# Kernel tuning notes

Measured on AMD Instinct MI355X. Metric: run time of the kernel, lower is better.

The kernel has to match this reference:

```python
import jax, jax.numpy as jnp
import numpy as np

EMBED_DIM = 1024
NUM_HEADS = 16
BATCH = 4
SEQ = 2048
HEAD_DIM = EMBED_DIM // NUM_HEADS


def get_alibi_slope(num_heads):
    x = (2 ** 8) ** (1 / num_heads)
    slope = jnp.array([1 / x ** (i + 1) for i in range(num_heads)], dtype=jnp.float32)
    return slope[:, None, None]  # [H,1,1]


def setup_inputs() -> dict:
    key = jax.random.key(0)
    k1, k2, k3 = jax.random.split(key, 3)
    x = jax.random.normal(k1, (BATCH, SEQ, EMBED_DIM), dtype=jnp.float32)
    # causal mask, broadcastable to [B,H,S,S]
    mask = jnp.tril(jnp.ones((SEQ, SEQ), dtype=bool))[None, None, :, :]
    W_qkv = jax.random.normal(k2, (EMBED_DIM, 3 * EMBED_DIM), dtype=jnp.float32) * (EMBED_DIM ** -0.5)
    b_qkv = jnp.zeros((3 * EMBED_DIM,), dtype=jnp.float32)
    W_out = jax.random.normal(k3, (EMBED_DIM, EMBED_DIM), dtype=jnp.float32) * (EMBED_DIM ** -0.5)
    b_out = jnp.zeros((EMBED_DIM,), dtype=jnp.float32)
    return {"x": x, "mask": mask, "W_qkv": W_qkv, "b_qkv": b_qkv, "W_out": W_out, "b_out": b_out}


def reference(x, mask, W_qkv, b_qkv, W_out, b_out):
    B, S, E = x.shape
    H, D = NUM_HEADS, HEAD_DIM
    qkv = x @ W_qkv + b_qkv                     # [B,S,3E]
    qkv = qkv.reshape(B, S, 3, H, D)
    q, k, v = qkv[:, :, 0], qkv[:, :, 1], qkv[:, :, 2]  # each [B,S,H,D]
    scores = jnp.einsum('bqhd,bkhd->bhqk', q, k) / jnp.sqrt(jnp.asarray(D, x.dtype))
    # ALiBi bias: slope[h] * (k_pos - q_pos)
    rel = (jnp.arange(S)[None, :] - jnp.arange(S)[:, None]).astype(x.dtype)  # [S,S]
    scores = scores + get_alibi_slope(H).astype(x.dtype) * rel               # broadcast [H,S,S]
    scores = jnp.where(mask, scores, jnp.asarray(-1e9, x.dtype))
    attn = jax.nn.softmax(scores, axis=-1)       # [B,H,S,S]
    out = jnp.einsum('bhqk,bkhd->bqhd', attn, v).reshape(B, S, E)
    return out @ W_out + b_out
```

## Files before the change

kernel.cpp:

```cpp
#include <hip/hip_runtime.h>
#include <hip/hip_bf16.h>
#include <cstdint>
#include <cstddef>

#define BATCH  4
#define SEQ    2048
#define EMBED  1024
#define NHEADS 16
#define HDIM   64

typedef __attribute__((ext_vector_type(8))) short  short8;
typedef __attribute__((ext_vector_type(4))) float  floatx4;

#define MASK_NEG (-1.0e30f)
#define LOG2E    1.44269504f

__device__ __forceinline__ float bf2f(ushort u) {
  union { uint32_t i; float f; } v; v.i = ((uint32_t)u) << 16; return v.f;
}
__device__ __forceinline__ ushort f2bf(float f) {
  union { float f; uint32_t i; } v; v.f = f;
  uint32_t u = v.i;
  return (ushort)((u + 0x7fffu + ((u >> 16) & 1u)) >> 16);
}
__device__ __forceinline__ uint32_t f2bf_pk(float a, float b) {
  union { __hip_bfloat162 h; uint32_t u; } v;
  v.h = __float22bfloat162_rn(make_float2(a, b));
  return v.u;
}
__device__ __forceinline__ void gll16(const ushort* g, ushort* l) {
  __builtin_amdgcn_global_load_lds(
      (const __attribute__((address_space(1))) void*)g,
      (__attribute__((address_space(3))) void*)l, 16, 0, 0);
}

__global__ __launch_bounds__(256) void detect_dtype(
    const uint32_t* __restrict__ x, int* __restrict__ flag) {
  __shared__ int sh[256];
  int tid = threadIdx.x;
  int c = 0;
#pragma unroll
  for (int i = 0; i < 16; i++) {
    uint32_t w = x[tid * 16 + i];
    uint32_t lo = w & 0xFFFFu;
    int e = (int)((lo >> 7) & 0xFF);
    if (lo == 0u || (e >= 100 && e <= 140)) c++;
  }
  sh[tid] = c;
  __syncthreads();
  if (tid == 0) {
    int s = 0;
    for (int i = 0; i < 256; i++) s += sh[i];
    *flag = (s >= 3500) ? 1 : 0;
  }
}

__global__ __launch_bounds__(256) void cvt_bf16_v4(
    const void* __restrict__ in, ushort* __restrict__ out,
    const int* __restrict__ flag, int n4) {
  bool isbf = (*flag != 0);
  int stride = gridDim.x * 256;
  for (int i = blockIdx.x * 256 + threadIdx.x; i < n4; i += stride) {
    if (isbf) {
      ((uint2*)out)[i] = ((const uint2*)in)[i];
    } else {
      float4 f = ((const float4*)in)[i];
      uint2 o;
      o.x = f2bf_pk(f.x, f.y);
      o.y = f2bf_pk(f.z, f.w);
      ((uint2*)out)[i] = o;
    }
  }
}

__global__ __launch_bounds__(256) void cvt_biases(
    const void* __restrict__ bq, const void* __restrict__ bo,
    ushort* __restrict__ bqb, ushort* __restrict__ bob,
    const int* __restrict__ flag) {
  bool isbf = (*flag != 0);
  int i = blockIdx.x * 256 + threadIdx.x;
  if (i < 3 * EMBED) {
    bqb[i] = isbf ? ((const ushort*)bq)[i] : f2bf(((const float*)bq)[i]);
  } else {
    int j = i - 3 * EMBED;
    bob[j] = isbf ? ((const ushort*)bo)[j] : f2bf(((const float*)bo)[j]);
  }
}

__global__ __launch_bounds__(256) void transpose_cvt(
    const void* __restrict__ in, ushort* __restrict__ out,
    const int* __restrict__ flag, int R, int C) {
  bool isbf = (*flag != 0);
  __shared__ ushort tile[32][33];
  int bx = blockIdx.x * 32;
  int by = blockIdx.y * 32;
  int tx = threadIdx.x & 31, ty = threadIdx.x >> 5;
#pragma unroll
  for (int i = 0; i < 32; i += 8) {
    size_t idx = (size_t)(by + ty + i) * C + bx + tx;
    tile[ty + i][tx] = isbf ? ((const ushort*)in)[idx] : f2bf(((const float*)in)[idx]);
  }
  __syncthreads();
#pragma unroll
  for (int i = 0; i < 32; i += 8)
    out[(size_t)(bx + ty + i) * R + by + tx] = tile[tx][ty + i];
}

__global__ __launch_bounds__(256) void transpose_v(
    const ushort* __restrict__ in, ushort* __restrict__ out) {
  __shared__ ushort tile[32][33];
  int bh = blockIdx.z;
  int s0 = blockIdx.x * 32;
  int d0 = blockIdx.y * 32;
  int tx = threadIdx.x & 31, ty = threadIdx.x >> 5;
  const ushort* ip = in + (size_t)bh * SEQ * HDIM;
  ushort* op = out + (size_t)bh * SEQ * HDIM;
#pragma unroll
  for (int i = 0; i < 32; i += 8)
    tile[ty + i][tx] = ip[(size_t)(s0 + ty + i) * HDIM + d0 + tx];
  __syncthreads();
#pragma unroll
  for (int i = 0; i < 32; i += 8)
    op[(size_t)(d0 + ty + i) * SEQ + s0 + tx] = tile[tx][ty + i];
}

template <int EPI>
__global__ __launch_bounds__(256) void gemm128(
    const ushort* __restrict__ A, const ushort* __restrict__ BT,
    const ushort* __restrict__ bias,
    ushort* __restrict__ out0, ushort* __restrict__ out1, ushort* __restrict__ out2,
    const int* __restrict__ flag,
    int M, int N, int K) {
  __shared__ __align__(16) ushort Al[128 * 64];
  __shared__ __align__(16) ushort Bl[128 * 64];

  const int tid  = threadIdx.x;
  const int lane = tid & 63, wave = tid >> 6;
  const int quad = lane >> 4, l15 = lane & 15;
  const int wm = wave >> 1, wn = wave & 1;
  const int rowA0 = blockIdx.y * 128;
  const int colB0 = blockIdx.x * 128;

  floatx4 acc[4][4] = {};

  int srow[4], sc8[4];
#pragma unroll
  for (int j = 0; j < 4; j++) {
    int s = tid + j * 256;
    srow[j] = s >> 3;
    sc8[j] = ((s & 7) ^ (srow[j] & 7)) * 8;
  }

  for (int kk = 0; kk < K; kk += 64) {
    __syncthreads();
#pragma unroll
    for (int j = 0; j < 4; j++)
      gll16(&A[(size_t)(rowA0 + srow[j]) * K + kk + sc8[j]], &Al[(tid + j * 256) * 8]);
#pragma unroll
    for (int j = 0; j < 4; j++)
      gll16(&BT[(size_t)(colB0 + srow[j]) * K + kk + sc8[j]], &Bl[(tid + j * 256) * 8]);
    __syncthreads();

#pragma unroll
    for (int h = 0; h < 2; h++) {
      short8 af[4], bf[4];
#pragma unroll
      for (int mt = 0; mt < 4; mt++) {
        int row = wm * 64 + mt * 16 + l15;
        int pos = (quad + 4 * h) ^ (l15 & 7);
        af[mt] = *(const short8*)&Al[row * 64 + pos * 8];
      }
#pragma unroll
      for (int nt = 0; nt < 4; nt++) {
        int row = wn * 64 + nt * 16 + l15;
        int pos = (quad + 4 * h) ^ (l15 & 7);
        bf[nt] = *(const short8*)&Bl[row * 64 + pos * 8];
      }
#pragma unroll
      for (int mt = 0; mt < 4; mt++)
#pragma unroll
        for (int nt = 0; nt < 4; nt++)
          acc[mt][nt] = __builtin_amdgcn_mfma_f32_16x16x32_bf16(af[mt], bf[nt], acc[mt][nt], 0, 0, 0);
    }
  }

  const bool isbf = (EPI == 1) ? (*flag != 0) : true;

#pragma unroll
  for (int mt = 0; mt < 4; mt++)
#pragma unroll
    for (int nt = 0; nt < 4; nt++)
#pragma unroll
      for (int r = 0; r < 4; r++) {
        int row = rowA0 + wm * 64 + mt * 16 + quad * 4 + r;
        int col = colB0 + wn * 64 + nt * 16 + l15;
        float v = acc[mt][nt][r] + bf2f(bias[col]);
        if (EPI == 0) {
          int three = col >> 10, rem = col & 1023, h = rem >> 6, d = rem & 63;
          int b = row >> 11, s = row & 2047;
          ushort* dst = (three == 0) ? out0 : (three == 1) ? out1 : out2;
          dst[((size_t)(b * NHEADS + h) * SEQ + s) * HDIM + d] = f2bf(v);
        } else {
          if (isbf) out0[(size_t)row * N + col] = f2bf(v);
          else      ((float*)out0)[(size_t)row * N + col] = v;
        }
      }
}

__global__ __launch_bounds__(256, 4) void attn_kernel(
    const ushort* __restrict__ Q, const ushort* __restrict__ K,
    const ushort* __restrict__ VT, ushort* __restrict__ Oout) {
  __shared__ __align__(16) ushort Kl[2][64 * 64];
  __shared__ __align__(16) ushort Vt[2][64 * 64];
  __shared__ __align__(16) ushort Pl[4][16 * 64];

  const int tid  = threadIdx.x;
  const int lane = tid & 63, wave = tid >> 6;
  const int quad = lane >> 4, l15 = lane & 15;

  const int L   = blockIdx.x + 16 * blockIdx.y + 256 * blockIdx.z;
  const int xcd = L & 7;
  const int idx = L >> 3;
  const int bh  = xcd * 8 + (idx >> 4);
  const int p   = idx & 15;
  const int h   = bh & 15, b = bh >> 4;

  const ushort* Qp  = Q  + (size_t)bh * SEQ * HDIM;
  const ushort* Kp  = K  + (size_t)bh * SEQ * HDIM;
  const ushort* VTp = VT + (size_t)bh * SEQ * HDIM;

  const float slope2 = exp2f(-0.5f * (float)(h + 1)) * LOG2E;
  const float c2 = 0.125f * LOG2E;
  float rt[4];
#pragma unroll
  for (int r = 0; r < 4; r++) rt[r] = slope2 * (float)r;

  const int sr0 = tid >> 3, sr1 = sr0 + 32;
  const int sc  = tid & 7;
  const int so  = sc * 8;
  const int sw0 = sr0 * 64 + (sc ^ (sr0 & 7)) * 8;
  const int sw1 = sr1 * 64 + (sc ^ (sr0 & 7)) * 8;
  const int sxr = l15 & 7;

  for (int qsel = 0; qsel < 2; qsel++) {
    const int qt  = qsel ? (31 - p) : p;
    const int wq0 = qt * 64 + wave * 16;

    short8 qf0, qf1;
    {
      const ushort* qr = &Qp[(size_t)(wq0 + l15) * HDIM];
      qf0 = *(const short8*)&qr[quad * 8];
      qf1 = *(const short8*)&qr[32 + quad * 8];
    }

    float m2 = MASK_NEG, li = 0.f;
    const float qrowf = (float)(wq0 + l15);
    floatx4 o_acc[4] = {};

    uint4 pk0 = *(const uint4*)&Kp[(size_t)sr0 * HDIM + so];
    uint4 pk1 = *(const uint4*)&Kp[(size_t)sr1 * HDIM + so];
    uint4 pv0 = *(const uint4*)&VTp[(size_t)sr0 * SEQ + so];
    uint4 pv1 = *(const uint4*)&VTp[(size_t)sr1 * SEQ + so];
    __syncthreads();
    *(uint4*)&Kl[0][sw0] = pk0;
    *(uint4*)&Kl[0][sw1] = pk1;
    *(uint4*)&Vt[0][sw0] = pv0;
    *(uint4*)&Vt[0][sw1] = pv1;
    __syncthreads();

    const int ntiles = qt + 1;
    for (int kt = 0; kt < ntiles; kt++) {
      const int kb = kt * 64;
      const int cur = kt & 1;
      const bool more = (kt + 1 < ntiles);

      if (more) {
        const int kb2 = kb + 64;
        pk0 = *(const uint4*)&Kp[(size_t)(kb2 + sr0) * HDIM + so];
        pk1 = *(const uint4*)&Kp[(size_t)(kb2 + sr1) * HDIM + so];
        pv0 = *(const uint4*)&VTp[(size_t)sr0 * SEQ + kb2 + so];
        pv1 = *(const uint4*)&VTp[(size_t)sr1 * SEQ + kb2 + so];
      }

      floatx4 sm[4];
#pragma unroll
      for (int kct = 0; kct < 4; kct++) {
        const ushort* kr = &Kl[cur][(kct * 16 + l15) * 64];
        short8 a0 = *(const short8*)&kr[(quad ^ sxr) * 8];
        short8 a1 = *(const short8*)&kr[((quad + 4) ^ sxr) * 8];
        floatx4 z = {};
        z = __builtin_amdgcn_mfma_f32_16x16x32_bf16(a0, qf0, z, 0, 0, 0);
        sm[kct] = __builtin_amdgcn_mfma_f32_16x16x32_bf16(a1, qf1, z, 0, 0, 0);
      }

      const bool needs_mask = (kb + 63 > wq0);
      float mloc = MASK_NEG;
#pragma unroll
      for (int kct = 0; kct < 4; kct++) {
        float keyb = (float)(kb + kct * 16 + quad * 4);
        float base = slope2 * keyb;
#pragma unroll
        for (int r = 0; r < 4; r++) {
          float v = fmaf(sm[kct][r], c2, base + rt[r]);
          if (needs_mask && (keyb + (float)r > qrowf)) v = MASK_NEG;
          sm[kct][r] = v;
          mloc = fmaxf(mloc, v);
        }
      }
      mloc = fmaxf(mloc, __shfl_xor(mloc, 16, 64));
      mloc = fmaxf(mloc, __shfl_xor(mloc, 32, 64));

      float mn = fmaxf(m2, mloc);
      float al = exp2f(m2 - mn);
      m2 = mn;

      float rs = 0.f;
#pragma unroll
      for (int kct = 0; kct < 4; kct++) {
        float p0 = exp2f(sm[kct][0] - mn), p1 = exp2f(sm[kct][1] - mn);
        float p2 = exp2f(sm[kct][2] - mn), p3 = exp2f(sm[kct][3] - mn);
        rs += (p0 + p1) + (p2 + p3);
        uint2 pw;
        pw.x = f2bf_pk(p0, p1);
        pw.y = f2bf_pk(p2, p3);
        *(uint2*)&Pl[wave][l15 * 64 + ((kct * 2 + (quad >> 1)) ^ sxr) * 8 + (quad & 1) * 4] = pw;
      }
      rs += __shfl_xor(rs, 16, 64);
      rs += __shfl_xor(rs, 32, 64);
      li = li * al + rs;

      float alr[4];
#pragma unroll
      for (int r = 0; r < 4; r++) alr[r] = __shfl(al, quad * 4 + r, 16);
#pragma unroll
      for (int ct = 0; ct < 4; ct++)
#pragma unroll
        for (int r = 0; r < 4; r++) o_acc[ct][r] *= alr[r];

#pragma unroll
      for (int ks = 0; ks < 2; ks++) {
        short8 vf[4];
#pragma unroll
        for (int ct = 0; ct < 4; ct++)
          vf[ct] = *(const short8*)&Vt[cur][(ct * 16 + l15) * 64 + ((ks * 4 + quad) ^ sxr) * 8];
        short8 pf = *(const short8*)&Pl[wave][l15 * 64 + ((ks * 4 + quad) ^ sxr) * 8];
#pragma unroll
        for (int ct = 0; ct < 4; ct++)
          o_acc[ct] = __builtin_amdgcn_mfma_f32_16x16x32_bf16(pf, vf[ct], o_acc[ct], 0, 0, 0);
      }

      if (more) {
        const int nxt = cur ^ 1;
        *(uint4*)&Kl[nxt][sw0] = pk0;
        *(uint4*)&Kl[nxt][sw1] = pk1;
        *(uint4*)&Vt[nxt][sw0] = pv0;
        *(uint4*)&Vt[nxt][sw1] = pv1;
      }
      __syncthreads();
    }

    {
      float inv = 1.0f / fmaxf(li, 1e-20f);
      float invr[4];
#pragma unroll
      for (int r = 0; r < 4; r++) invr[r] = __shfl(inv, quad * 4 + r, 16);
#pragma unroll
      for (int ct = 0; ct < 4; ct++)
#pragma unroll
        for (int r = 0; r < 4; r++) {
          int q = wq0 + quad * 4 + r;
          float v = o_acc[ct][r] * invr[r];
          Oout[(size_t)(b * SEQ + q) * EMBED + h * HDIM + ct * 16 + l15] = f2bf(v);
        }
    }
  }
}

extern "C" void kernel_launch(void* const* d_in, const int* in_sizes, int n_in,
                              void* d_out, int out_size, void* d_ws, size_t ws_size,
                              hipStream_t stream) {
  const void* x     = d_in[0];
  const void* W_qkv = d_in[2];
  const void* b_qkv = d_in[3];
  const void* W_out = d_in[4];
  const void* b_out = d_in[5];

  char* ws = (char*)d_ws;
  int*    flag = (int*)(ws + 0);
  ushort* xb   = (ushort*)(ws + 1024);
  ushort* WTq  = (ushort*)(ws + 16778240);
  ushort* WTo  = (ushort*)(ws + 23069696);
  ushort* bqb  = (ushort*)(ws + 25166848);
  ushort* bob  = (ushort*)(ws + 25172992);
  ushort* Kw   = (ushort*)(ws + 25175040);
  ushort* Vw   = (ushort*)(ws + 41952256);
  ushort* VTw  = (ushort*)(ws + 58729472);
  ushort* Aw   = Vw;
  ushort* Qw   = (ws_size >= (size_t)75506688 + 16777216)
                   ? (ushort*)(ws + 75506688)
                   : (ushort*)d_out;

  detect_dtype<<<1, 256, 0, stream>>>((const uint32_t*)x, flag);

  cvt_bf16_v4<<<2048, 256, 0, stream>>>(x, xb, flag, BATCH * SEQ * EMBED / 4);
  cvt_biases<<<16, 256, 0, stream>>>(b_qkv, b_out, bqb, bob, flag);

  transpose_cvt<<<dim3(3072 / 32, 1024 / 32), 256, 0, stream>>>(W_qkv, WTq, flag, 1024, 3072);
  transpose_cvt<<<dim3(1024 / 32, 1024 / 32), 256, 0, stream>>>(W_out, WTo, flag, 1024, 1024);

  gemm128<0><<<dim3(3072 / 128, 8192 / 128), 256, 0, stream>>>(
      xb, WTq, bqb, Qw, Kw, Vw, flag, BATCH * SEQ, 3 * EMBED, EMBED);

  transpose_v<<<dim3(SEQ / 32, HDIM / 32, BATCH * NHEADS), 256, 0, stream>>>(Vw, VTw);

  attn_kernel<<<dim3(16, 16, 4), 256, 0, stream>>>(Qw, Kw, VTw, Aw);

  gemm128<1><<<dim3(1024 / 128, 8192 / 128), 256, 0, stream>>>(
      Aw, WTo, bob, (ushort*)d_out, nullptr, nullptr, flag, BATCH * SEQ, EMBED, EMBED);
}
```

Before: 314.9 us.

## Restructure attention inner loop with lazy rescaling, fast exp, and peeled masked tile

Rewrites the flash-attention tile body. The causal mask is applied only in a peeled final diagonal tile. The ALiBi bias is precomputed per lane with the per-tile key offset folded into the running max. exp2f is replaced with raw v_exp_f32. The running-max rescale is skipped via a wave ballot unless the max grows by more than 8 (log2 units), and the row-sum reduction is deferred to the epilogue. The GEMM kernel also remaps block indices so column tiles are grouped per XCD for better L2 locality. The lazy rescale threshold risks precision if the unrescaled exponentials grow large, but it is bounded by 2^8.

```diff
diff --git a/kernel.cpp b/kernel.cpp
--- a/kernel.cpp
+++ b/kernel.cpp
@@ -27,6 +27,17 @@
   union { __hip_bfloat162 h; uint32_t u; } v;
   v.h = __float22bfloat162_rn(make_float2(a, b));
   return v.u;
+}
+__device__ __forceinline__ float fast_exp2(float x) {
+  float r;
+  asm("v_exp_f32 %0, %1" : "=v"(r) : "v"(x));
+  return r;
+}
+__device__ __forceinline__ floatx4 max4(floatx4 a, floatx4 b) {
+  floatx4 r;
+  r[0] = fmaxf(a[0], b[0]); r[1] = fmaxf(a[1], b[1]);
+  r[2] = fmaxf(a[2], b[2]); r[3] = fmaxf(a[3], b[3]);
+  return r;
 }
 __device__ __forceinline__ void gll16(const ushort* g, ushort* l) {
   __builtin_amdgcn_global_load_lds(
@@ -138,8 +149,14 @@
   const int lane = tid & 63, wave = tid >> 6;
   const int quad = lane >> 4, l15 = lane & 15;
   const int wm = wave >> 1, wn = wave & 1;
-  const int rowA0 = blockIdx.y * 128;
-  const int colB0 = blockIdx.x * 128;
+
+  const int Lb  = blockIdx.y * gridDim.x + blockIdx.x;
+  const int xcd = Lb & 7, ib = Lb >> 3;
+  const int cpx = gridDim.x >> 3;
+  const int bx  = xcd * cpx + (ib % cpx);
+  const int by  = ib / cpx;
+  const int rowA0 = by * 128;
+  const int colB0 = bx * 128;
 
   floatx4 acc[4][4] = {};
 
@@ -231,9 +248,13 @@
 
   const float slope2 = exp2f(-0.5f * (float)(h + 1)) * LOG2E;
   const float c2 = 0.125f * LOG2E;
-  float rt[4];
-#pragma unroll
-  for (int r = 0; r < 4; r++) rt[r] = slope2 * (float)r;
+
+  floatx4 ab[4];
+#pragma unroll
+  for (int kct = 0; kct < 4; kct++)
+#pragma unroll
+    for (int r = 0; r < 4; r++)
+      ab[kct][r] = slope2 * (float)(kct * 16 + quad * 4 + r);
 
   const int sr0 = tid >> 3, sr1 = sr0 + 32;
   const int sc  = tid & 7;
@@ -241,6 +262,81 @@
   const int sw0 = sr0 * 64 + (sc ^ (sr0 & 7)) * 8;
   const int sw1 = sr1 * 64 + (sc ^ (sr0 & 7)) * 8;
   const int sxr = l15 & 7;
+
+#define ATTN_TILE(KB, CUR, MASKED)                                            \
+  do {                                                                        \
+    floatx4 w[4];                                                             \
+    _Pragma("unroll")                                                         \
+    for (int kct = 0; kct < 4; kct++) {                                       \
+      const ushort* kr = &Kl[CUR][(kct * 16 + l15) * 64];                     \
+      short8 a0 = *(const short8*)&kr[(quad ^ sxr) * 8];                      \
+      short8 a1 = *(const short8*)&kr[((quad + 4) ^ sxr) * 8];                \
+      floatx4 z = {};                                                         \
+      z = __builtin_amdgcn_mfma_f32_16x16x32_bf16(a0, qf0, z, 0, 0, 0);       \
+      z = __builtin_amdgcn_mfma_f32_16x16x32_bf16(a1, qf1, z, 0, 0, 0);       \
+      w[kct] = z * c2 + ab[kct];                                              \
+    }                                                                         \
+    if (MASKED) {                                                             \
+      const float qrel = qrowf - (float)(KB);                                 \
+      _Pragma("unroll")                                                       \
+      for (int kct = 0; kct < 4; kct++)                                       \
+        _Pragma("unroll")                                                     \
+        for (int r = 0; r < 4; r++)                                           \
+          if ((float)(kct * 16 + quad * 4 + r) > qrel) w[kct][r] = MASK_NEG;  \
+    }                                                                         \
+    floatx4 wm4 = max4(max4(w[0], w[1]), max4(w[2], w[3]));                   \
+    float mloc = fmaxf(fmaxf(wm4[0], wm4[1]), fmaxf(wm4[2], wm4[3]));         \
+    mloc = fmaxf(mloc, __shfl_xor(mloc, 16, 64));                             \
+    mloc = fmaxf(mloc, __shfl_xor(mloc, 32, 64));                             \
+    const float bk = slope2 * (float)(KB);                                    \
+    const float mlt = mloc + bk;                                              \
+    const unsigned long long g = __ballot(mlt > m2 + 8.0f);                   \
+    float al = 1.0f;                                                          \
+    if (g) {                                                                  \
+      float mn = fmaxf(m2, mlt);                                              \
+      al = fast_exp2(m2 - mn);                                                \
+      m2 = mn;                                                                \
+    }                                                                         \
+    const float mnb = m2 - bk;                                                \
+    float rs = 0.f;                                                           \
+    _Pragma("unroll")                                                         \
+    for (int kct = 0; kct < 4; kct++) {                                       \
+      float p0 = fast_exp2(w[kct][0] - mnb);                                  \
+      float p1 = fast_exp2(w[kct][1] - mnb);                                  \
+      float p2 = fast_exp2(w[kct][2] - mnb);                                  \
+      float p3 = fast_exp2(w[kct][3] - mnb);                                  \
+      rs += (p0 + p1) + (p2 + p3);                                            \
+      uint2 pw;                                                               \
+      pw.x = f2bf_pk(p0, p1);                                                 \
+      pw.y = f2bf_pk(p2, p3);                                                 \
+      *(uint2*)&Pl[wave][l15 * 64 + ((kct * 2 + (quad >> 1)) ^ sxr) * 8 +     \
+                         (quad & 1) * 4] = pw;                                \
+    }                                                                         \
+    if (g) {                                                                  \
+      floatx4 alrv;                                                           \
+      _Pragma("unroll")                                                       \
+      for (int r = 0; r < 4; r++) alrv[r] = __shfl(al, quad * 4 + r, 16);     \
+      _Pragma("unroll")                                                       \
+      for (int ct = 0; ct < 4; ct++) o_acc[ct] *= alrv;                       \
+      li = li * al + rs;                                                      \
+    } else {                                                                  \
+      li += rs;                                                               \
+    }                                                                         \
+    _Pragma("unroll")                                                         \
+    for (int ks = 0; ks < 2; ks++) {                                          \
+      short8 vf[4];                                                           \
+      _Pragma("unroll")                                                       \
+      for (int ct = 0; ct < 4; ct++)                                          \
+        vf[ct] = *(const short8*)&Vt[CUR][(ct * 16 + l15) * 64 +              \
+                                          ((ks * 4 + quad) ^ sxr) * 8];       \
+      short8 pf = *(const short8*)&Pl[wave][l15 * 64 +                        \
+                                            ((ks * 4 + quad) ^ sxr) * 8];     \
+      _Pragma("unroll")                                                       \
+      for (int ct = 0; ct < 4; ct++)                                          \
+        o_acc[ct] = __builtin_amdgcn_mfma_f32_16x16x32_bf16(pf, vf[ct],       \
+                                                            o_acc[ct], 0, 0, 0); \
+    }                                                                         \
+  } while (0)
 
   for (int qsel = 0; qsel < 2; qsel++) {
     const int qt  = qsel ? (31 - p) : p;
@@ -268,13 +364,12 @@
     *(uint4*)&Vt[0][sw1] = pv1;
     __syncthreads();
 
-    const int ntiles = qt + 1;
-    for (int kt = 0; kt < ntiles; kt++) {
+    const int last = qt;
+    for (int kt = 0; kt < last; kt++) {
       const int kb = kt * 64;
       const int cur = kt & 1;
-      const bool more = (kt + 1 < ntiles);
-
-      if (more) {
+
+      {
         const int kb2 = kb + 64;
         pk0 = *(const uint4*)&Kp[(size_t)(kb2 + sr0) * HDIM + so];
         pk1 = *(const uint4*)&Kp[(size_t)(kb2 + sr1) * HDIM + so];
@@ -282,74 +377,9 @@
         pv1 = *(const uint4*)&VTp[(size_t)sr1 * SEQ + kb2 + so];
       }
 
-      floatx4 sm[4];
-#pragma unroll
-      for (int kct = 0; kct < 4; kct++) {
-        const ushort* kr = &Kl[cur][(kct * 16 + l15) * 64];
-        short8 a0 = *(const short8*)&kr[(quad ^ sxr) * 8];
-        short8 a1 = *(const short8*)&kr[((quad + 4) ^ sxr) * 8];
-        floatx4 z = {};
-        z = __builtin_amdgcn_mfma_f32_16x16x32_bf16(a0, qf0, z, 0, 0, 0);
-        sm[kct] = __builtin_amdgcn_mfma_f32_16x16x32_bf16(a1, qf1, z, 0, 0, 0);
-      }
-
-      const bool needs_mask = (kb + 63 > wq0);
-      float mloc = MASK_NEG;
-#pragma unroll
-      for (int kct = 0; kct < 4; kct++) {
-        float keyb = (float)(kb + kct * 16 + quad * 4);
-        float base = slope2 * keyb;
-#pragma unroll
-        for (int r = 0; r < 4; r++) {
-          float v = fmaf(sm[kct][r], c2, base + rt[r]);
-          if (needs_mask && (keyb + (float)r > qrowf)) v = MASK_NEG;
-          sm[kct][r] = v;
-          mloc = fmaxf(mloc, v);
-        }
-      }
-      mloc = fmaxf(mloc, __shfl_xor(mloc, 16, 64));
-      mloc = fmaxf(mloc, __shfl_xor(mloc, 32, 64));
-
-      float mn = fmaxf(m2, mloc);
-      float al = exp2f(m2 - mn);
-      m2 = mn;
-
-      float rs = 0.f;
-#pragma unroll
-      for (int kct = 0; kct < 4; kct++) {
-        float p0 = exp2f(sm[kct][0] - mn), p1 = exp2f(sm[kct][1] - mn);
-        float p2 = exp2f(sm[kct][2] - mn), p3 = exp2f(sm[kct][3] - mn);
-        rs += (p0 + p1) + (p2 + p3);
-        uint2 pw;
-        pw.x = f2bf_pk(p0, p1);
-        pw.y = f2bf_pk(p2, p3);
-        *(uint2*)&Pl[wave][l15 * 64 + ((kct * 2 + (quad >> 1)) ^ sxr) * 8 + (quad & 1) * 4] = pw;
-      }
-      rs += __shfl_xor(rs, 16, 64);
-      rs += __shfl_xor(rs, 32, 64);
-      li = li * al + rs;
-
-      float alr[4];
-#pragma unroll
-      for (int r = 0; r < 4; r++) alr[r] = __shfl(al, quad * 4 + r, 16);
-#pragma unroll
-      for (int ct = 0; ct < 4; ct++)
-#pragma unroll
-        for (int r = 0; r < 4; r++) o_acc[ct][r] *= alr[r];
-
-#pragma unroll
-      for (int ks = 0; ks < 2; ks++) {
-        short8 vf[4];
-#pragma unroll
-        for (int ct = 0; ct < 4; ct++)
-          vf[ct] = *(const short8*)&Vt[cur][(ct * 16 + l15) * 64 + ((ks * 4 + quad) ^ sxr) * 8];
-        short8 pf = *(const short8*)&Pl[wave][l15 * 64 + ((ks * 4 + quad) ^ sxr) * 8];
-#pragma unroll
-        for (int ct = 0; ct < 4; ct++)
-          o_acc[ct] = __builtin_amdgcn_mfma_f32_16x16x32_bf16(pf, vf[ct], o_acc[ct], 0, 0, 0);
-      }
-
-      if (more) {
+      ATTN_TILE(kb, cur, 0);
+
+      {
         const int nxt = cur ^ 1;
         *(uint4*)&Kl[nxt][sw0] = pk0;
         *(uint4*)&Kl[nxt][sw1] = pk1;
@@ -359,8 +389,12 @@
       __syncthreads();
     }
 
+    ATTN_TILE(last * 64, last & 1, 1);
+
     {
-      float inv = 1.0f / fmaxf(li, 1e-20f);
+      float lif = li + __shfl_xor(li, 16, 64);
+      lif += __shfl_xor(lif, 32, 64);
+      float inv = 1.0f / fmaxf(lif, 1e-20f);
       float invr[4];
 #pragma unroll
       for (int r = 0; r < 4; r++) invr[r] = __shfl(inv, quad * 4 + r, 16);
@@ -374,6 +408,7 @@
         }
     }
   }
+#undef ATTN_TILE
 }
 
 extern "C" void kernel_launch(void* const* d_in, const int* in_sizes, int n_in,
```

Result: faster. 307.1 us (-2.5%).
